# Optimization experiments

Measured on AMD Instinct MI355X. Metric: run time of the kernel, lower is better.

## Reference

```python
import jax, jax.numpy as jnp
import numpy as np
from jax import lax

B, D, N, C = 8, 1, 12288, 256
H = 8            # num_heads
WS = 64          # window size (pixels per window)
HID = 1024       # mlp hidden = 4*C
K = 9            # conv kernel size
EPS = 1e-5


def setup_inputs() -> dict:
    key = jax.random.key(0)
    ks = jax.random.split(key, 8)
    w = lambda i, shape: jax.random.normal(ks[i], shape, jnp.float32) * 0.02
    return {
        "x": jax.random.normal(ks[0], (B, D, N, C), jnp.float32),
        "ln1_g": jnp.ones((C,), jnp.float32),
        "ln1_b": jnp.zeros((C,), jnp.float32),
        "conv_w": w(1, (C, C, K)),            # OIH layout (out_ch, in_ch, k)
        "conv_b": jnp.zeros((C,), jnp.float32),
        "qkv_w": w(2, (C, 3 * C)),            # stored (in, out): y = x @ W + b
        "qkv_b": jnp.zeros((3 * C,), jnp.float32),
        "proj_w": w(3, (C, C)),
        "proj_b": jnp.zeros((C,), jnp.float32),
        "ln2_g": jnp.ones((C,), jnp.float32),
        "ln2_b": jnp.zeros((C,), jnp.float32),
        "fc1_w": w(4, (C, HID)),
        "fc1_b": jnp.zeros((HID,), jnp.float32),
        "fc2_w": w(5, (HID, C)),
        "fc2_b": jnp.zeros((C,), jnp.float32),
    }


def _layernorm(x, g, b):
    mu = jnp.mean(x, axis=-1, keepdims=True)
    var = jnp.mean(jnp.square(x - mu), axis=-1, keepdims=True)
    return (x - mu) * lax.rsqrt(var + EPS) * g + b


def reference(x, ln1_g, ln1_b, conv_w, conv_b, qkv_w, qkv_b,
              proj_w, proj_b, ln2_g, ln2_b, fc1_w, fc1_b, fc2_w, fc2_b):
    shortcut = x                                  # (B, D, N, C)
    h = _layernorm(x, ln1_g, ln1_b)

    # Conv1d over pixel dim N, channels C, same padding
    hc = h.reshape(B * D, N, C).transpose(0, 2, 1)            # (BD, C, N)
    hc = lax.conv_general_dilated(
        hc, conv_w, window_strides=(1,), padding=[((K - 1) // 2, (K - 1) // 2)],
        dimension_numbers=("NCH", "OIH", "NCH"))
    hc = hc + conv_b[None, :, None]
    h = hc.transpose(0, 2, 1).reshape(B, D, N, C)

    # Window partition (no shift): (B*D*N/WS, WS, C)
    win = h.reshape(-1, WS, C)
    hd = C // H
    qkv = (win @ qkv_w + qkv_b).reshape(-1, WS, 3, H, hd)
    q = qkv[:, :, 0].transpose(0, 2, 1, 3)        # (nW, H, WS, hd)
    k = qkv[:, :, 1].transpose(0, 2, 1, 3)
    v = qkv[:, :, 2].transpose(0, 2, 1, 3)
    scale = hd ** (-0.5)
    attn = jnp.einsum("whqd,whkd->whqk", q * scale, k)
    attn = jax.nn.softmax(attn, axis=-1)
    out = jnp.einsum("whqk,whkd->whqd", attn, v)
    out = out.transpose(0, 2, 1, 3).reshape(-1, WS, C)
    out = out @ proj_w + proj_b

    h = out.reshape(B, D, N, C)
    x1 = shortcut + h                             # residual 1
    mlp_in = _layernorm(x1, ln2_g, ln2_b)
    mlp = jax.nn.gelu(mlp_in @ fc1_w + fc1_b, approximate=False) @ fc2_w + fc2_b
    return x1 + mlp                               # residual 2
```

## Files before the change

kernel.cpp:

```cpp
#include <hip/hip_runtime.h>

#define DEVI __device__ __forceinline__

typedef __attribute__((ext_vector_type(4))) float  f32x4;
typedef __attribute__((ext_vector_type(8))) short  s16x8;
typedef __attribute__((ext_vector_type(4))) short  s16x4;
typedef __attribute__((ext_vector_type(8))) __bf16 bf16x8;

constexpr int  Nn  = 12288;
constexpr int  NP  = 12296;
constexpr long TOK = 98304;

DEVI short f2bf(float f) {
  unsigned u = __builtin_bit_cast(unsigned, f);
  u += 0x7fffu + ((u >> 16) & 1u);
  return (short)(u >> 16);
}

DEVI f32x4 MFMA(s16x8 a, s16x8 b, f32x4 c) {
  return __builtin_amdgcn_mfma_f32_16x16x32_bf16(
      __builtin_bit_cast(bf16x8, a), __builtin_bit_cast(bf16x8, b), c, 0, 0, 0);
}

DEVI void gld16(const void* g, void* l) {
  __builtin_amdgcn_global_load_lds(
      (const __attribute__((address_space(1))) void*)g,
      (__attribute__((address_space(3))) void*)l, 16, 0, 0);
}

template <int UNITS>
DEVI void stage64(const short* __restrict__ g_base, long g_row0, int ld, int k0,
                  short* __restrict__ lds, int w, int lane) {
#pragma unroll
  for (int cc = 0; cc < UNITS; ++cc) {
    const int u = cc * 256 + w * 64 + lane;
    const int row = u >> 3, ch = u & 7;
    const short* g = g_base + (g_row0 + row) * (long)ld + k0 + ch * 8;
    gld16(g, lds + (cc * 256 + w * 64) * 8);
  }
}

DEVI void xcd_decode(int W, int total, int ncol, long& row0, int& col0) {
  const int per = total >> 3;
  const int L = (W & 7) * per + (W >> 3);
  row0 = (long)(L / ncol) * 128;
  col0 = (L % ncol) * 128;
}

__global__ void prep_k(const float* __restrict__ qkv_w, const float* __restrict__ proj_w,
                       const float* __restrict__ fc1_w, const float* __restrict__ fc2_w,
                       const float* __restrict__ conv_w,
                       short* __restrict__ qkvWt, short* __restrict__ projWt,
                       short* __restrict__ fc1Wt, short* __restrict__ fc2Wt,
                       short* __restrict__ convWt, short* __restrict__ hp) {
  int idx = blockIdx.x * 256 + threadIdx.x;
  if (idx < 196608) {
    int o = idx >> 8, i = idx & 255;
    qkvWt[idx] = f2bf(qkv_w[i * 768 + o]);
    return;
  }
  idx -= 196608;
  if (idx < 65536) {
    int o = idx >> 8, i = idx & 255;
    projWt[idx] = f2bf(proj_w[i * 256 + o]);
    return;
  }
  idx -= 65536;
  if (idx < 262144) {
    int o = idx >> 8, i = idx & 255;
    fc1Wt[idx] = f2bf(fc1_w[i * 1024 + o]);
    return;
  }
  idx -= 262144;
  if (idx < 262144) {
    int o = idx >> 10, i = idx & 1023;
    fc2Wt[idx] = f2bf(fc2_w[i * 256 + o]);
    return;
  }
  idx -= 262144;
  if (idx < 589824) {
    int co = idx / 2304, rem = idx % 2304;
    int k = rem >> 8, ci = rem & 255;
    convWt[idx] = f2bf(conv_w[co * 2304 + ci * 9 + k]);
    return;
  }
  idx -= 589824;
  if (idx < 16384) {
    int b = idx >> 11, rem = idx & 2047;
    int rs = rem >> 8, ch = rem & 255;
    int p = rs < 4 ? rs : 12288 + rs;
    hp[((long)b * NP + p) * 256 + ch] = 0;
  }
}

__global__ __launch_bounds__(256) void ln_k(const float* __restrict__ x,
                                            const float* __restrict__ gw,
                                            const float* __restrict__ bw,
                                            short* __restrict__ out) {
  const int tid = threadIdx.x, w = tid >> 6, lane = tid & 63;
  const long t = (long)blockIdx.x * 4 + w;
  f32x4 v = *((const f32x4*)(x + t * 256) + lane);
  float s  = v[0] + v[1] + v[2] + v[3];
  float ss = v[0] * v[0] + v[1] * v[1] + v[2] * v[2] + v[3] * v[3];
#pragma unroll
  for (int mk = 1; mk < 64; mk <<= 1) {
    s  += __shfl_xor(s, mk);
    ss += __shfl_xor(ss, mk);
  }
  const float mu   = s * (1.0f / 256.0f);
  const float var  = ss * (1.0f / 256.0f) - mu * mu;
  const float rstd = rsqrtf(var + 1e-5f);
  f32x4 g4 = *((const f32x4*)gw + lane);
  f32x4 b4 = *((const f32x4*)bw + lane);
  const long orow = t + (t / Nn) * 8 + 4;
  s16x4 o4;
#pragma unroll
  for (int j = 0; j < 4; ++j) o4[j] = f2bf((v[j] - mu) * rstd * g4[j] + b4[j]);
  *((s16x4*)(out + orow * 256) + lane) = o4;
}

template <int EPI>
__global__ __launch_bounds__(256, 2) void gemm_k(
    const short* __restrict__ A, int lda,
    const short* __restrict__ Bt,
    const float* __restrict__ bias,
    const float* res, short* outS, float* outF,
    int ldo, int K, int ncol) {
  __shared__ __align__(16) short As[128][64];
  __shared__ __align__(16) short Bs[128][64];
  const int tid = threadIdx.x, w = tid >> 6, lane = tid & 63;
  const int q = lane >> 4, r16 = lane & 15;
  long row0; int col0;
  xcd_decode(blockIdx.x, gridDim.x, ncol, row0, col0);
  const int wr = w >> 1, wc = w & 1;
  f32x4 acc[4][4] = {};

  for (int k0 = 0; k0 < K; k0 += 64) {
    stage64<4>(A, row0, lda, k0, &As[0][0], w, lane);
    stage64<4>(Bt, col0, K, k0, &Bs[0][0], w, lane);
    __syncthreads();
#pragma unroll
    for (int kk = 0; kk < 2; ++kk) {
      s16x8 af[4], bfv[4];
#pragma unroll
      for (int m = 0; m < 4; ++m) af[m] = *(const s16x8*)&As[wr * 64 + m * 16 + r16][kk * 32 + q * 8];
#pragma unroll
      for (int n = 0; n < 4; ++n) bfv[n] = *(const s16x8*)&Bs[wc * 64 + n * 16 + r16][kk * 32 + q * 8];
#pragma unroll
      for (int m = 0; m < 4; ++m)
#pragma unroll
        for (int n = 0; n < 4; ++n) acc[m][n] = MFMA(af[m], bfv[n], acc[m][n]);
    }
    __syncthreads();
  }

  const long orow = row0 + wr * 64;
  const int  ocol = col0 + wc * 64;
#pragma unroll
  for (int n = 0; n < 4; ++n) {
    const int   gc = ocol + n * 16 + r16;
    const float bn = bias[gc];
#pragma unroll
    for (int m = 0; m < 4; ++m) {
      const long gr = orow + m * 16 + q * 4;
#pragma unroll
      for (int r = 0; r < 4; ++r) {
        float v = acc[m][n][r] + bn;
        const long o = (gr + r) * (long)ldo + gc;
        if constexpr (EPI == 0) {
          outS[o] = f2bf(v);
        } else if constexpr (EPI == 1) {
          outF[o] = v + res[o];
        } else {
          float t = 0.5f * v * (1.0f + erff(v * 0.70710678118654752f));
          outS[o] = f2bf(t);
        }
      }
    }
  }
}

__global__ __launch_bounds__(256, 2) void conv_k(const short* __restrict__ hp,
                                                 const short* __restrict__ convWt,
                                                 const float* __restrict__ bias,
                                                 short* __restrict__ out) {
  __shared__ __align__(16) short As[160][64];
  __shared__ __align__(16) short Bs[128][64];
  const int tid = threadIdx.x, w = tid >> 6, lane = tid & 63;
  const int q = lane >> 4, r16 = lane & 15;
  long row0; int col0;
  xcd_decode(blockIdx.x, gridDim.x, 2, row0, col0);
  const int  b  = (int)(row0 / Nn);
  const int  n0 = (int)(row0 % Nn);
  const long abase = (long)b * NP + n0;
  const int  wr = w >> 1, wc = w & 1;
  f32x4 acc[4][4] = {};

  for (int k0 = 0; k0 < 256; k0 += 64) {
    stage64<5>(hp, abase, 256, k0, &As[0][0], w, lane);
    for (int tap = 0; tap < 9; ++tap) {
      stage64<4>(convWt, col0, 2304, tap * 256 + k0, &Bs[0][0], w, lane);
      __syncthreads();
#pragma unroll
      for (int kk = 0; kk < 2; ++kk) {
        s16x8 af[4], bfv[4];
#pragma unroll
        for (int m = 0; m < 4; ++m)
          af[m] = *(const s16x8*)&As[tap + wr * 64 + m * 16 + r16][kk * 32 + q * 8];
#pragma unroll
        for (int n = 0; n < 4; ++n)
          bfv[n] = *(const s16x8*)&Bs[wc * 64 + n * 16 + r16][kk * 32 + q * 8];
#pragma unroll
        for (int m = 0; m < 4; ++m)
#pragma unroll
          for (int n = 0; n < 4; ++n) acc[m][n] = MFMA(af[m], bfv[n], acc[m][n]);
      }
      __syncthreads();
    }
  }

  const long orow = row0 + wr * 64;
  const int  ocol = col0 + wc * 64;
#pragma unroll
  for (int n = 0; n < 4; ++n) {
    const int   gc = ocol + n * 16 + r16;
    const float bn = bias[gc];
#pragma unroll
    for (int m = 0; m < 4; ++m) {
      const long gr = orow + m * 16 + q * 4;
#pragma unroll
      for (int r = 0; r < 4; ++r) out[(gr + r) * 256L + gc] = f2bf(acc[m][n][r] + bn);
    }
  }
}

__global__ __launch_bounds__(256, 2) void proj_ln_k(
    const short* __restrict__ A,
    const short* __restrict__ Bt,
    const float* __restrict__ bias,
    const float* __restrict__ res,
    const float* __restrict__ gw, const float* __restrict__ bw,
    float* __restrict__ x1,
    short* __restrict__ lnout) {
  __shared__ __align__(16) short As[128][64];
  __shared__ __align__(16) short Bs[256][64];
  __shared__ float red[2][128][2];
  const int tid = threadIdx.x, w = tid >> 6, lane = tid & 63;
  const int q = lane >> 4, r16 = lane & 15;
  const int W = blockIdx.x, per = gridDim.x >> 3;
  const long row0 = (long)((W & 7) * per + (W >> 3)) * 128;
  const int wr = w >> 1, wc = w & 1;
  f32x4 acc[4][8] = {};

  for (int k0 = 0; k0 < 256; k0 += 64) {
    stage64<4>(A, row0, 256, k0, &As[0][0], w, lane);
    stage64<8>(Bt, 0, 256, k0, &Bs[0][0], w, lane);
    __syncthreads();
#pragma unroll
    for (int kk = 0; kk < 2; ++kk) {
      s16x8 af[4], bfv[8];
#pragma unroll
      for (int m = 0; m < 4; ++m) af[m] = *(const s16x8*)&As[wr * 64 + m * 16 + r16][kk * 32 + q * 8];
#pragma unroll
      for (int n = 0; n < 8; ++n) bfv[n] = *(const s16x8*)&Bs[wc * 128 + n * 16 + r16][kk * 32 + q * 8];
#pragma unroll
      for (int m = 0; m < 4; ++m)
#pragma unroll
        for (int n = 0; n < 8; ++n) acc[m][n] = MFMA(af[m], bfv[n], acc[m][n]);
    }
    __syncthreads();
  }

  float s[4][4] = {}, ss[4][4] = {};
#pragma unroll
  for (int n = 0; n < 8; ++n) {
    const int   gc = wc * 128 + n * 16 + r16;
    const float bn = bias[gc];
#pragma unroll
    for (int m = 0; m < 4; ++m) {
#pragma unroll
      for (int r = 0; r < 4; ++r) {
        const long gr = row0 + wr * 64 + m * 16 + q * 4 + r;
        float v = acc[m][n][r] + bn + res[gr * 256 + gc];
        acc[m][n][r] = v;
        x1[gr * 256 + gc] = v;
        s[m][r] += v;
        ss[m][r] += v * v;
      }
    }
  }
#pragma unroll
  for (int m = 0; m < 4; ++m)
#pragma unroll
    for (int r = 0; r < 4; ++r) {
#pragma unroll
      for (int mk = 1; mk < 16; mk <<= 1) {
        s[m][r]  += __shfl_xor(s[m][r], mk);
        ss[m][r] += __shfl_xor(ss[m][r], mk);
      }
      if (r16 == 0) {
        const int lr = wr * 64 + m * 16 + q * 4 + r;
        red[wc][lr][0] = s[m][r];
        red[wc][lr][1] = ss[m][r];
      }
    }
  __syncthreads();
#pragma unroll
  for (int m = 0; m < 4; ++m)
#pragma unroll
    for (int r = 0; r < 4; ++r) {
      const int  lr = wr * 64 + m * 16 + q * 4 + r;
      const long gr = row0 + lr;
      const float S  = red[0][lr][0] + red[1][lr][0];
      const float SS = red[0][lr][1] + red[1][lr][1];
      const float mu = S * (1.0f / 256.0f);
      const float rstd = rsqrtf(SS * (1.0f / 256.0f) - mu * mu + 1e-5f);
#pragma unroll
      for (int n = 0; n < 8; ++n) {
        const int gc = wc * 128 + n * 16 + r16;
        lnout[gr * 256 + gc] = f2bf((acc[m][n][r] - mu) * rstd * gw[gc] + bw[gc]);
      }
    }
}

__global__ __launch_bounds__(256, 2) void attn_k(const short* __restrict__ qkv,
                                                 short* __restrict__ o) {
  __shared__ __align__(16) short Pt[4][64][68];
  __shared__ __align__(16) short Vs[4][64][32];
  const int tid = threadIdx.x, w = tid >> 6, lane = tid & 63;
  const int q = lane >> 4, r16 = lane & 15;
  const int job = blockIdx.x * 4 + w;
  const int win = job >> 3, h = job & 7;
  const short* base = qkv + (long)win * 64 * 768;

#pragma unroll
  for (int c = 0; c < 4; ++c) {
    const int idx16 = c * 64 + lane;
    const short* g = base + (long)(idx16 >> 2) * 768 + 512 + h * 32 + (idx16 & 3) * 8;
    gld16(g, (char*)&Vs[w][0][0] + c * 1024);
  }

  s16x8 aq[4], bk[4];
#pragma unroll
  for (int m = 0; m < 4; ++m)
    aq[m] = *(const s16x8*)(base + (long)(m * 16 + r16) * 768 + h * 32 + q * 8);
#pragma unroll
  for (int n = 0; n < 4; ++n)
    bk[n] = *(const s16x8*)(base + (long)(n * 16 + r16) * 768 + 256 + h * 32 + q * 8);
  f32x4 sc[4][4] = {};
#pragma unroll
  for (int m = 0; m < 4; ++m)
#pragma unroll
    for (int n = 0; n < 4; ++n) sc[m][n] = MFMA(aq[m], bk[n], sc[m][n]);

  const float scale = 0.17677669529663687f;
#pragma unroll
  for (int m = 0; m < 4; ++m) {
#pragma unroll
    for (int r = 0; r < 4; ++r) {
      float a0 = sc[m][0][r] * scale, a1 = sc[m][1][r] * scale;
      float a2 = sc[m][2][r] * scale, a3 = sc[m][3][r] * scale;
      float mx = fmaxf(fmaxf(a0, a1), fmaxf(a2, a3));
      mx = fmaxf(mx, __shfl_xor(mx, 1));
      mx = fmaxf(mx, __shfl_xor(mx, 2));
      mx = fmaxf(mx, __shfl_xor(mx, 4));
      mx = fmaxf(mx, __shfl_xor(mx, 8));
      float e0 = __expf(a0 - mx), e1 = __expf(a1 - mx);
      float e2 = __expf(a2 - mx), e3 = __expf(a3 - mx);
      float sm = e0 + e1 + e2 + e3;
      sm += __shfl_xor(sm, 1);
      sm += __shfl_xor(sm, 2);
      sm += __shfl_xor(sm, 4);
      sm += __shfl_xor(sm, 8);
      float inv = 1.0f / sm;
      sc[m][0][r] = e0 * inv; sc[m][1][r] = e1 * inv;
      sc[m][2][r] = e2 * inv; sc[m][3][r] = e3 * inv;
    }
  }

#pragma unroll
  for (int m = 0; m < 4; ++m)
#pragma unroll
    for (int n = 0; n < 4; ++n) {
      s16x4 p4;
#pragma unroll
      for (int r = 0; r < 4; ++r) p4[r] = f2bf(sc[m][n][r]);
      *(s16x4*)&Pt[w][n * 16 + r16][m * 16 + q * 4] = p4;
    }

  asm volatile("s_waitcnt vmcnt(0)" ::: "memory");

  f32x4 oa[4][2] = {};
#pragma unroll
  for (int ks = 0; ks < 2; ++ks) {
    s16x8 bv[2];
#pragma unroll
    for (int nt = 0; nt < 2; ++nt)
#pragma unroll
      for (int jj = 0; jj < 8; ++jj)
        bv[nt][jj] = Vs[w][ks * 32 + q * 8 + jj][nt * 16 + r16];
#pragma unroll
    for (int m = 0; m < 4; ++m) {
      s16x8 ap;
#pragma unroll
      for (int jj = 0; jj < 8; ++jj)
        ap[jj] = Pt[w][ks * 32 + q * 8 + jj][m * 16 + r16];
#pragma unroll
      for (int nt = 0; nt < 2; ++nt) oa[m][nt] = MFMA(ap, bv[nt], oa[m][nt]);
    }
  }

  short* ob = o + (long)win * 64 * 256 + h * 32;
#pragma unroll
  for (int m = 0; m < 4; ++m)
#pragma unroll
    for (int nt = 0; nt < 2; ++nt)
#pragma unroll
      for (int r = 0; r < 4; ++r)
        ob[(long)(m * 16 + q * 4 + r) * 256 + nt * 16 + r16] = f2bf(oa[m][nt][r]);
}

extern "C" void kernel_launch(void* const* d_in, const int* in_sizes, int n_in,
                              void* d_out, int out_size, void* d_ws, size_t ws_size,
                              hipStream_t stream) {
  const float* x      = (const float*)d_in[0];
  const float* ln1_g  = (const float*)d_in[1];
  const float* ln1_b  = (const float*)d_in[2];
  const float* conv_w = (const float*)d_in[3];
  const float* conv_b = (const float*)d_in[4];
  const float* qkv_w  = (const float*)d_in[5];
  const float* qkv_b  = (const float*)d_in[6];
  const float* proj_w = (const float*)d_in[7];
  const float* proj_b = (const float*)d_in[8];
  const float* ln2_g  = (const float*)d_in[9];
  const float* ln2_b  = (const float*)d_in[10];
  const float* fc1_w  = (const float*)d_in[11];
  const float* fc1_b  = (const float*)d_in[12];
  const float* fc2_w  = (const float*)d_in[13];
  const float* fc2_b  = (const float*)d_in[14];
  float* out = (float*)d_out;

  constexpr long HPsz = (long)8 * NP * 256;
  constexpr long Qsz  = TOK * 768;
  constexpr long Csz  = TOK * 256;
  short* ws    = (short*)d_ws;
  short* hp    = ws;
  short* qkvB  = ws + HPsz;
  short* cvB   = ws + HPsz + Qsz;
  short* hidB  = qkvB;
  short* wts   = ws + HPsz + Qsz + Csz;
  short* qkvWt  = wts;
  short* projWt = qkvWt + 196608;
  short* fc1Wt  = projWt + 65536;
  short* fc2Wt  = fc1Wt + 262144;
  short* convWt = fc2Wt + 262144;

  prep_k<<<5440, 256, 0, stream>>>(qkv_w, proj_w, fc1_w, fc2_w, conv_w,
                                   qkvWt, projWt, fc1Wt, fc2Wt, convWt, hp);
  ln_k<<<24576, 256, 0, stream>>>(x, ln1_g, ln1_b, hp);
  conv_k<<<1536, 256, 0, stream>>>(hp, convWt, conv_b, cvB);
  gemm_k<0><<<4608, 256, 0, stream>>>(cvB, 256, qkvWt, qkv_b,
                                      nullptr, qkvB, nullptr, 768, 256, 6);
  attn_k<<<3072, 256, 0, stream>>>(qkvB, hp);
  proj_ln_k<<<768, 256, 0, stream>>>(hp, projWt, proj_b, x, ln2_g, ln2_b, out, hp);
  gemm_k<2><<<6144, 256, 0, stream>>>(hp, 256, fc1Wt, fc1_b,
                                      nullptr, hidB, nullptr, 1024, 256, 8);
  gemm_k<1><<<1536, 256, 0, stream>>>(hidB, 1024, fc2Wt, fc2_b,
                                      out, nullptr, out, 256, 1024, 2);
}
```

Baseline: 671.3 us.

## Double-buffer LDS staging in GEMM and conv; widen proj_ln to 8 warps

The GEMM and conv kernels now use two LDS buffers, so the next K-slice (or next conv tap's weights) is loaded while MFMAs run on the current one, with one barrier per step instead of two. The proj+LayerNorm kernel moves from 4 to 8 waves per block, giving each wave a 64x64 tile and cutting accumulator registers, which should raise occupancy. The price is doubled LDS use, which may lower occupancy in the GEMM kernels. Also, the async global-to-LDS loads are only ordered by the single barrier at the end of each step.

```diff
diff --git a/kernel.cpp b/kernel.cpp
--- a/kernel.cpp
+++ b/kernel.cpp
@@ -28,15 +28,16 @@
       (__attribute__((address_space(3))) void*)l, 16, 0, 0);
 }
 
-template <int UNITS>
-DEVI void stage64(const short* __restrict__ g_base, long g_row0, int ld, int k0,
-                  short* __restrict__ lds, int w, int lane) {
-#pragma unroll
-  for (int cc = 0; cc < UNITS; ++cc) {
-    const int u = cc * 256 + w * 64 + lane;
+template <int CNT, int NT>
+DEVI void stageG(const short* __restrict__ g_base, long g_row0, int ld, int k0,
+                 short* __restrict__ lds, int tid) {
+  const int w = tid >> 6;
+#pragma unroll
+  for (int c = 0; c < CNT; ++c) {
+    const int u = c * NT + tid;
     const int row = u >> 3, ch = u & 7;
     const short* g = g_base + (g_row0 + row) * (long)ld + k0 + ch * 8;
-    gld16(g, lds + (cc * 256 + w * 64) * 8);
+    gld16(g, lds + (c * NT + w * 64) * 8);
   }
 }
 
@@ -126,8 +127,8 @@
     const float* __restrict__ bias,
     const float* res, short* outS, float* outF,
     int ldo, int K, int ncol) {
-  __shared__ __align__(16) short As[128][64];
-  __shared__ __align__(16) short Bs[128][64];
+  __shared__ __align__(16) short As[2][128][64];
+  __shared__ __align__(16) short Bs[2][128][64];
   const int tid = threadIdx.x, w = tid >> 6, lane = tid & 63;
   const int q = lane >> 4, r16 = lane & 15;
   long row0; int col0;
@@ -135,23 +136,29 @@
   const int wr = w >> 1, wc = w & 1;
   f32x4 acc[4][4] = {};
 
+  stageG<4, 256>(A, row0, lda, 0, &As[0][0][0], tid);
+  stageG<4, 256>(Bt, col0, K, 0, &Bs[0][0][0], tid);
+  __syncthreads();
+  int cur = 0;
   for (int k0 = 0; k0 < K; k0 += 64) {
-    stage64<4>(A, row0, lda, k0, &As[0][0], w, lane);
-    stage64<4>(Bt, col0, K, k0, &Bs[0][0], w, lane);
-    __syncthreads();
+    if (k0 + 64 < K) {
+      stageG<4, 256>(A, row0, lda, k0 + 64, &As[cur ^ 1][0][0], tid);
+      stageG<4, 256>(Bt, col0, K, k0 + 64, &Bs[cur ^ 1][0][0], tid);
+    }
 #pragma unroll
     for (int kk = 0; kk < 2; ++kk) {
       s16x8 af[4], bfv[4];
 #pragma unroll
-      for (int m = 0; m < 4; ++m) af[m] = *(const s16x8*)&As[wr * 64 + m * 16 + r16][kk * 32 + q * 8];
-#pragma unroll
-      for (int n = 0; n < 4; ++n) bfv[n] = *(const s16x8*)&Bs[wc * 64 + n * 16 + r16][kk * 32 + q * 8];
+      for (int m = 0; m < 4; ++m) af[m] = *(const s16x8*)&As[cur][wr * 64 + m * 16 + r16][kk * 32 + q * 8];
+#pragma unroll
+      for (int n = 0; n < 4; ++n) bfv[n] = *(const s16x8*)&Bs[cur][wc * 64 + n * 16 + r16][kk * 32 + q * 8];
 #pragma unroll
       for (int m = 0; m < 4; ++m)
 #pragma unroll
         for (int n = 0; n < 4; ++n) acc[m][n] = MFMA(af[m], bfv[n], acc[m][n]);
     }
     __syncthreads();
+    cur ^= 1;
   }
 
   const long orow = row0 + wr * 64;
@@ -185,7 +192,7 @@
                                                  const float* __restrict__ bias,
                                                  short* __restrict__ out) {
   __shared__ __align__(16) short As[160][64];
-  __shared__ __align__(16) short Bs[128][64];
+  __shared__ __align__(16) short Bs[2][128][64];
   const int tid = threadIdx.x, w = tid >> 6, lane = tid & 63;
   const int q = lane >> 4, r16 = lane & 15;
   long row0; int col0;
@@ -196,11 +203,16 @@
   const int  wr = w >> 1, wc = w & 1;
   f32x4 acc[4][4] = {};
 
+  stageG<5, 256>(hp, abase, 256, 0, &As[0][0], tid);
+  stageG<4, 256>(convWt, col0, 2304, 0, &Bs[0][0][0], tid);
+  __syncthreads();
+  int cur = 0;
   for (int k0 = 0; k0 < 256; k0 += 64) {
-    stage64<5>(hp, abase, 256, k0, &As[0][0], w, lane);
     for (int tap = 0; tap < 9; ++tap) {
-      stage64<4>(convWt, col0, 2304, tap * 256 + k0, &Bs[0][0], w, lane);
-      __syncthreads();
+      if (tap < 8)
+        stageG<4, 256>(convWt, col0, 2304, (tap + 1) * 256 + k0, &Bs[cur ^ 1][0][0], tid);
+      else if (k0 + 64 < 256)
+        stageG<4, 256>(convWt, col0, 2304, k0 + 64, &Bs[cur ^ 1][0][0], tid);
 #pragma unroll
       for (int kk = 0; kk < 2; ++kk) {
         s16x8 af[4], bfv[4];
@@ -209,12 +221,17 @@
           af[m] = *(const s16x8*)&As[tap + wr * 64 + m * 16 + r16][kk * 32 + q * 8];
 #pragma unroll
         for (int n = 0; n < 4; ++n)
-          bfv[n] = *(const s16x8*)&Bs[wc * 64 + n * 16 + r16][kk * 32 + q * 8];
+          bfv[n] = *(const s16x8*)&Bs[cur][wc * 64 + n * 16 + r16][kk * 32 + q * 8];
 #pragma unroll
         for (int m = 0; m < 4; ++m)
 #pragma unroll
           for (int n = 0; n < 4; ++n) acc[m][n] = MFMA(af[m], bfv[n], acc[m][n]);
       }
+      __syncthreads();
+      cur ^= 1;
+    }
+    if (k0 + 64 < 256) {
+      stageG<5, 256>(hp, abase, 256, k0 + 64, &As[0][0], tid);
       __syncthreads();
     }
   }
@@ -234,7 +251,7 @@
   }
 }
 
-__global__ __launch_bounds__(256, 2) void proj_ln_k(
+__global__ __launch_bounds__(512, 4) void proj_ln_k(
     const short* __restrict__ A,
     const short* __restrict__ Bt,
     const float* __restrict__ bias,
@@ -244,83 +261,85 @@
     short* __restrict__ lnout) {
   __shared__ __align__(16) short As[128][64];
   __shared__ __align__(16) short Bs[256][64];
-  __shared__ float red[2][128][2];
+  __shared__ float red[4][128][2];
   const int tid = threadIdx.x, w = tid >> 6, lane = tid & 63;
   const int q = lane >> 4, r16 = lane & 15;
   const int W = blockIdx.x, per = gridDim.x >> 3;
   const long row0 = (long)((W & 7) * per + (W >> 3)) * 128;
-  const int wr = w >> 1, wc = w & 1;
-  f32x4 acc[4][8] = {};
+  const int wr = w >> 2, wc = w & 3;
+  f32x4 acc[4][4] = {};
 
   for (int k0 = 0; k0 < 256; k0 += 64) {
-    stage64<4>(A, row0, 256, k0, &As[0][0], w, lane);
-    stage64<8>(Bt, 0, 256, k0, &Bs[0][0], w, lane);
+    stageG<2, 512>(A, row0, 256, k0, &As[0][0], tid);
+    stageG<4, 512>(Bt, 0, 256, k0, &Bs[0][0], tid);
     __syncthreads();
 #pragma unroll
     for (int kk = 0; kk < 2; ++kk) {
-      s16x8 af[4], bfv[8];
+      s16x8 af[4], bfv[4];
 #pragma unroll
       for (int m = 0; m < 4; ++m) af[m] = *(const s16x8*)&As[wr * 64 + m * 16 + r16][kk * 32 + q * 8];
 #pragma unroll
-      for (int n = 0; n < 8; ++n) bfv[n] = *(const s16x8*)&Bs[wc * 128 + n * 16 + r16][kk * 32 + q * 8];
+      for (int n = 0; n < 4; ++n) bfv[n] = *(const s16x8*)&Bs[wc * 64 + n * 16 + r16][kk * 32 + q * 8];
 #pragma unroll
       for (int m = 0; m < 4; ++m)
 #pragma unroll
-        for (int n = 0; n < 8; ++n) acc[m][n] = MFMA(af[m], bfv[n], acc[m][n]);
+        for (int n = 0; n < 4; ++n) acc[m][n] = MFMA(af[m], bfv[n], acc[m][n]);
     }
     __syncthreads();
   }
 
-  float s[4][4] = {}, ss[4][4] = {};
-#pragma unroll
-  for (int n = 0; n < 8; ++n) {
-    const int   gc = wc * 128 + n * 16 + r16;
-    const float bn = bias[gc];
-#pragma unroll
-    for (int m = 0; m < 4; ++m) {
-#pragma unroll
-      for (int r = 0; r < 4; ++r) {
-        const long gr = row0 + wr * 64 + m * 16 + q * 4 + r;
-        float v = acc[m][n][r] + bn + res[gr * 256 + gc];
+  float biasr[4], gv[4], bv[4];
+#pragma unroll
+  for (int n = 0; n < 4; ++n) {
+    const int gc = wc * 64 + n * 16 + r16;
+    biasr[n] = bias[gc]; gv[n] = gw[gc]; bv[n] = bw[gc];
+  }
+
+#pragma unroll
+  for (int m = 0; m < 4; ++m) {
+#pragma unroll
+    for (int r = 0; r < 4; ++r) {
+      const long gr = row0 + wr * 64 + m * 16 + q * 4 + r;
+      float s = 0.f, ss = 0.f;
+#pragma unroll
+      for (int n = 0; n < 4; ++n) {
+        const int gc = wc * 64 + n * 16 + r16;
+        float v = acc[m][n][r] + biasr[n] + res[gr * 256 + gc];
         acc[m][n][r] = v;
         x1[gr * 256 + gc] = v;
-        s[m][r] += v;
-        ss[m][r] += v * v;
-      }
-    }
-  }
-#pragma unroll
-  for (int m = 0; m < 4; ++m)
-#pragma unroll
-    for (int r = 0; r < 4; ++r) {
+        s += v; ss += v * v;
+      }
 #pragma unroll
       for (int mk = 1; mk < 16; mk <<= 1) {
-        s[m][r]  += __shfl_xor(s[m][r], mk);
-        ss[m][r] += __shfl_xor(ss[m][r], mk);
+        s  += __shfl_xor(s, mk);
+        ss += __shfl_xor(ss, mk);
       }
       if (r16 == 0) {
         const int lr = wr * 64 + m * 16 + q * 4 + r;
-        red[wc][lr][0] = s[m][r];
-        red[wc][lr][1] = ss[m][r];
-      }
-    }
+        red[wc][lr][0] = s;
+        red[wc][lr][1] = ss;
+      }
+    }
+  }
   __syncthreads();
-#pragma unroll
-  for (int m = 0; m < 4; ++m)
+
+#pragma unroll
+  for (int m = 0; m < 4; ++m) {
 #pragma unroll
     for (int r = 0; r < 4; ++r) {
       const int  lr = wr * 64 + m * 16 + q * 4 + r;
       const long gr = row0 + lr;
-      const float S  = red[0][lr][0] + red[1][lr][0];
-      const float SS = red[0][lr][1] + red[1][lr][1];
+      const float S  = red[0][lr][0] + red[1][lr][0] + red[2][lr][0] + red[3][lr][0];
+      const float SS = red[0][lr][1] + red[1][lr][1] + red[2][lr][1] + red[3][lr][1];
       const float mu = S * (1.0f / 256.0f);
       const float rstd = rsqrtf(SS * (1.0f / 256.0f) - mu * mu + 1e-5f);
 #pragma unroll
-      for (int n = 0; n < 8; ++n) {
-        const int gc = wc * 128 + n * 16 + r16;
-        lnout[gr * 256 + gc] = f2bf((acc[m][n][r] - mu) * rstd * gw[gc] + bw[gc]);
-      }
-    }
+      for (int n = 0; n < 4; ++n) {
+        const int gc = wc * 64 + n * 16 + r16;
+        lnout[gr * 256 + gc] = f2bf((acc[m][n][r] - mu) * rstd * gv[n] + bv[n]);
+      }
+    }
+  }
 }
 
 __global__ __launch_bounds__(256, 2) void attn_k(const short* __restrict__ qkv,
@@ -462,7 +481,7 @@
   gemm_k<0><<<4608, 256, 0, stream>>>(cvB, 256, qkvWt, qkv_b,
                                       nullptr, qkvB, nullptr, 768, 256, 6);
   attn_k<<<3072, 256, 0, stream>>>(qkvB, hp);
-  proj_ln_k<<<768, 256, 0, stream>>>(hp, projWt, proj_b, x, ln2_g, ln2_b, out, hp);
+  proj_ln_k<<<768, 512, 0, stream>>>(hp, projWt, proj_b, x, ln2_g, ln2_b, out, hp);
   gemm_k<2><<<6144, 256, 0, stream>>>(hp, 256, fc1Wt, fc1_b,
                                       nullptr, hidB, nullptr, 1024, 256, 8);
   gemm_k<1><<<1536, 256, 0, stream>>>(hidB, 1024, fc2Wt, fc2_b,
```

New measurement: 722.5 us. 1.08x slower.
